# Kernel optimization log

Measured on AMD Instinct MI355X. Metric: run time of the kernel, lower is better.

Reference implementation:

```python
import jax, jax.numpy as jnp
import numpy as np

V, E, H, D, DFF, NB, C, B, T = 32000, 512, 256, 512, 2048, 4, 16, 32, 512
PAD, BOS, EOS = 0, 1, 2


def positional_encoding(t, d):
    pos = jnp.arange(t, dtype=jnp.float32)[:, None]
    i = jnp.arange(0, d, 2, dtype=jnp.float32)
    div = jnp.exp(-(jnp.log(10000.0)) * i / d)
    pe = jnp.zeros((t, d), jnp.float32)
    pe = pe.at[:, 0::2].set(jnp.sin(pos * div))
    pe = pe.at[:, 1::2].set(jnp.cos(pos * div))
    return pe


def layernorm(x, g, b, eps=1e-5):
    mu = jnp.mean(x, -1, keepdims=True)
    var = jnp.mean((x - mu) ** 2, -1, keepdims=True)
    return (x - mu) * jax.lax.rsqrt(var + eps) * g + b


def gru_dir(xs, w_ih, w_hh, b_ih, b_hh, reverse):
    # xs: (B,T,E); precompute input projections for all t (one big GEMM)
    gi = jnp.einsum('bte,ge->btg', xs, w_ih) + b_ih  # (B,T,3H)
    h0 = jnp.zeros((xs.shape[0], H), xs.dtype)

    def step(h, gi_t):
        gh = h @ w_hh.T + b_hh
        i_r, i_z, i_n = jnp.split(gi_t, 3, -1)
        h_r, h_z, h_n = jnp.split(gh, 3, -1)
        r = jax.nn.sigmoid(i_r + h_r)
        z = jax.nn.sigmoid(i_z + h_z)
        n = jnp.tanh(i_n + r * h_n)
        h_new = (1.0 - z) * n + z * h
        return h_new, h_new

    _, hs = jax.lax.scan(step, h0, jnp.swapaxes(gi, 0, 1), reverse=reverse)
    return jnp.swapaxes(hs, 0, 1)  # (B,T,H)


def forward(x, y, embed_W, w_ih_f, w_hh_f, b_ih_f, b_hh_f, w_ih_b, w_hh_b, b_ih_b, b_hh_b,
            ff_w1, ff_b1, ff_w2, ff_b2, ln_g, ln_b, fc_w, fc_b, trans):
    h = embed_W[x]                                   # (B,T,E)
    h = h + positional_encoding(h.shape[1], E)[None]
    hf = gru_dir(h, w_ih_f, w_hh_f, b_ih_f, b_hh_f, False)
    hb = gru_dir(h, w_ih_b, w_hh_b, b_ih_b, b_hh_b, True)
    h = jnp.concatenate([hf, hb], -1)                # (B,T,D)
    for i in range(NB):                              # FeedForward blocks (residual + LN)
        ff = jax.nn.relu(h @ ff_w1[i] + ff_b1[i]) @ ff_w2[i] + ff_b2[i]
        h = layernorm(h + ff, ln_g[i], ln_b[i])
    logits = h @ fc_w + fc_b                         # (B,T,C) emissions

    # --- CRF viterbi decode ---
    mask = (y != PAD)                                # (B,T) bool
    emit = jnp.swapaxes(logits, 0, 1)                # (T,B,C)
    m = jnp.swapaxes(mask, 0, 1)                     # (T,B)
    score0 = trans[BOS][None] + emit[0]              # (B,C)

    def vstep(score, inp):
        e_t, m_t = inp                               # (B,C), (B,)
        cand = score[:, :, None] + trans[None] + e_t[:, None, :]  # (B,prev,cur)
        new = jnp.max(cand, axis=1)
        bp = jnp.argmax(cand, axis=1)                # (B,C)
        new = jnp.where(m_t[:, None], new, score)
        return new, bp

    final, bps = jax.lax.scan(vstep, score0, (emit[1:], m[1:]))  # bps: (T-1,B,C)
    final = final + trans[:, EOS][None]
    best_score = jnp.max(final, -1)                  # (B,)
    last_tag = jnp.argmax(final, -1)                 # (B,)

    def back(tag, inp):
        bp_t, m_t = inp
        prev = jnp.take_along_axis(bp_t, tag[:, None], axis=1)[:, 0]
        prev = jnp.where(m_t, prev, tag)
        return prev, tag

    first_tag, rest = jax.lax.scan(back, last_tag, (bps, m[1:]), reverse=True)
    path = jnp.swapaxes(jnp.concatenate([first_tag[None], rest], 0), 0, 1)  # (B,T)
    return best_score, path


def setup_inputs():
    key = jax.random.key(0)
    ks = jax.random.split(key, 16)
    nrm = lambda k, sh, sc: jax.random.normal(k, sh, jnp.float32) * sc
    s = 1.0 / float(np.sqrt(H))
    inp = {}
    inp['x'] = jax.random.randint(ks[0], (B, T), 1, V)
    inp['y'] = jax.random.randint(ks[1], (B, T), 0, 13) + 3  # in [3,16): no pad/bos/eos
    inp['embed_W'] = nrm(ks[2], (V, E), 0.02)
    inp['w_ih_f'] = nrm(ks[3], (3 * H, E), s); inp['w_hh_f'] = nrm(ks[4], (3 * H, H), s)
    inp['b_ih_f'] = nrm(ks[5], (3 * H,), s); inp['b_hh_f'] = nrm(ks[6], (3 * H,), s)
    inp['w_ih_b'] = nrm(ks[7], (3 * H, E), s); inp['w_hh_b'] = nrm(ks[8], (3 * H, H), s)
    inp['b_ih_b'] = nrm(ks[9], (3 * H,), s); inp['b_hh_b'] = nrm(ks[10], (3 * H,), s)
    inp['ff_w1'] = nrm(ks[11], (NB, D, DFF), 1.0 / float(np.sqrt(D)))
    inp['ff_b1'] = jnp.zeros((NB, DFF), jnp.float32)
    inp['ff_w2'] = nrm(ks[12], (NB, DFF, D), 1.0 / float(np.sqrt(DFF)))
    inp['ff_b2'] = jnp.zeros((NB, D), jnp.float32)
    inp['ln_g'] = jnp.ones((NB, D), jnp.float32); inp['ln_b'] = jnp.zeros((NB, D), jnp.float32)
    inp['fc_w'] = nrm(ks[13], (D, C), 1.0 / float(np.sqrt(D)))
    inp['fc_b'] = jnp.zeros((C,), jnp.float32)
    inp['trans'] = nrm(ks[14], (C, C), 0.1)
    return inp


def reference(x, y, embed_W, w_ih_f, w_hh_f, b_ih_f, b_hh_f, w_ih_b, w_hh_b, b_ih_b, b_hh_b,
              ff_w1, ff_b1, ff_w2, ff_b2, ln_g, ln_b, fc_w, fc_b, trans):
    return forward(x, y, embed_W, w_ih_f, w_hh_f, b_ih_f, b_hh_f, w_ih_b, w_hh_b, b_ih_b, b_hh_b,
                   ff_w1, ff_b1, ff_w2, ff_b2, ln_g, ln_b, fc_w, fc_b, trans)
```

## Files before the change

kernel.cpp:

```cpp
#include <hip/hip_runtime.h>

#define DEV __device__ __forceinline__

using short8 = __attribute__((ext_vector_type(8))) short;
using f32x4  = __attribute__((ext_vector_type(4))) float;
using i32x4  = __attribute__((ext_vector_type(4))) int;

DEV float b2f(short s) {
  union { unsigned u; float f; } c;
  c.u = ((unsigned)(unsigned short)s) << 16;
  return c.f;
}
DEV short f2b(float f) {
  union { float f; unsigned u; } c; c.f = f;
  unsigned u = c.u + 0x7fffu + ((c.u >> 16) & 1u);
  return (short)(u >> 16);
}
DEV float fast_sigmoid(float x) {
  return __builtin_amdgcn_rcpf(1.f + __expf(-x));
}
DEV float fast_tanh(float x) {
  return 1.f - 2.f * __builtin_amdgcn_rcpf(1.f + __expf(2.f * x));
}
DEV void async_ld16(const void* g, void* lds) {
  __builtin_amdgcn_global_load_lds(
      (const __attribute__((address_space(1))) void*)(unsigned long long)g,
      (__attribute__((address_space(3))) void*)(unsigned)(unsigned long long)lds,
      16, 0, 0);
}

__global__ __launch_bounds__(256) void k_cvt2(const float* __restrict__ a, const float* __restrict__ b,
                                              short* __restrict__ oa, short* __restrict__ ob) {
  int blk = blockIdx.x;
  const float* in; short* out; int base;
  if (blk < 384) { in = a; out = oa; base = blk; }
  else           { in = b; out = ob; base = blk - 384; }
  int i = base * 256 + threadIdx.x;
  f32x4 v = *(const f32x4*)(in + (size_t)i * 4);
  short4 o;
#pragma unroll
  for (int j = 0; j < 4; j++) ((short*)&o)[j] = f2b(v[j]);
  *(short4*)(out + (size_t)i * 4) = o;
}

__global__ __launch_bounds__(256) void k_wq8(const float* __restrict__ wf,
                                             const float* __restrict__ wb,
                                             int* __restrict__ out) {
  int flat = blockIdx.x * 256 + threadIdx.x;
  int lane = flat & 63;
  int c = (flat >> 6) & 3;
  int t = flat >> 8;
  int g = t % 3;
  int t2 = t / 3;
  int v = t2 & 15, d = t2 >> 4;
  const float* w = d ? wb : wf;
  int row = g * 256 + v * 16 + (lane & 15);
  int k0 = c * 64 + (lane >> 4) * 16;
  const float* p = w + (size_t)row * 256 + k0;
  int pk[4];
#pragma unroll
  for (int i = 0; i < 4; i++) {
    f32x4 f = *(const f32x4*)(p + i * 4);
    int b0 = (int)__builtin_rintf(f[0] * 256.f);
    int b1 = (int)__builtin_rintf(f[1] * 256.f);
    int b2 = (int)__builtin_rintf(f[2] * 256.f);
    int b3 = (int)__builtin_rintf(f[3] * 256.f);
    b0 = min(127, max(-127, b0)); b1 = min(127, max(-127, b1));
    b2 = min(127, max(-127, b2)); b3 = min(127, max(-127, b3));
    pk[i] = (b0 & 255) | ((b1 & 255) << 8) | ((b2 & 255) << 16) | ((b3 & 255) << 24);
  }
  *(int4*)(out + (size_t)flat * 4) = *(int4*)pk;
}

__global__ __launch_bounds__(256) void k_embed(const int* __restrict__ x,
                                               const float* __restrict__ W,
                                               short* __restrict__ h0) {
  int flat = blockIdx.x * 256 + threadIdx.x;
  int row  = flat >> 6;
  int e0   = (flat & 63) << 3;
  int tok  = x[row];
  int t    = row & 511;
  const float* wp = W + (size_t)tok * 512 + e0;
  float v[8];
  *(f32x4*)v       = *(const f32x4*)(wp);
  *(f32x4*)(v + 4) = *(const f32x4*)(wp + 4);
  short8 o;
#pragma unroll
  for (int i = 0; i < 8; i += 2) {
    float f = expf(-9.210340371976184f * (float)(e0 + i) * (1.f / 512.f));
    float ang = (float)t * f;
    o[i]     = f2b(v[i]     + sinf(ang));
    o[i + 1] = f2b(v[i + 1] + cosf(ang));
  }
  *(short8*)(h0 + (size_t)flat * 8) = o;
}

template <int MODE>
__global__ __launch_bounds__(256) void k_gemm(const short* __restrict__ A,
    const short* __restrict__ B, const float* __restrict__ bias,
    const float* __restrict__ bias2,
    float* __restrict__ Cf, short* __restrict__ Cb, int M, int N, int K,
    const float* __restrict__ tw1, const float* __restrict__ tw2,
    short* __restrict__ w1t, short* __restrict__ w2t) {
  __shared__ __align__(16) char smem[32768];
  short* smA = (short*)smem;
  short* smB = (short*)smem + 8192;
  const int blk0 = blockIdx.x;

  if (MODE == 3 && blk0 >= 1536) {
    int tileid = blk0 - 1536;
    const float* in; short* out; int R, C, tm;
    if (tileid < 4096) { int mat = tileid >> 10; in = tw1 + (size_t)mat * 1048576;
                         out = w1t + (size_t)mat * 1048576; R = 512; C = 2048; tm = tileid & 1023; }
    else               { int mat = (tileid - 4096) >> 10; in = tw2 + (size_t)mat * 1048576;
                         out = w2t + (size_t)mat * 1048576; R = 2048; C = 512; tm = tileid & 1023; }
    float (*tile)[33] = (float(*)[33])smem;
    int ct = C >> 5;
    int bc = tm % ct, br = tm / ct;
    int r0 = br << 5, c0 = bc << 5;
    for (int i = threadIdx.x; i < 1024; i += 256) {
      int r = i >> 5, c = i & 31;
      tile[r][c] = in[(size_t)(r0 + r) * C + c0 + c];
    }
    __syncthreads();
    for (int i = threadIdx.x; i < 1024; i += 256) {
      int c = i >> 5, r = i & 31;
      out[(size_t)(c0 + c) * R + r0 + r] = f2b(tile[r][c]);
    }
    return;
  }

  const int ngemm = (MODE == 3) ? 1536 : gridDim.x;
  const int blk = (blk0 % 8) * (ngemm >> 3) + (blk0 >> 3);
  const int tid = threadIdx.x, lane = tid & 63, wave = tid >> 6;
  const int m15 = lane & 15, quad = lane >> 4, q8 = quad << 3;
  const int tn = N >> 7;
  const int bm = blk / tn, bn = blk % tn;
  const int wm = wave & 1, wn = wave >> 1;
  const f32x4 z4 = {0.f, 0.f, 0.f, 0.f};
  f32x4 acc[4][4];
#pragma unroll
  for (int i = 0; i < 4; i++)
#pragma unroll
    for (int j = 0; j < 4; j++) acc[i][j] = z4;

  for (int k0 = 0; k0 < K; k0 += 64) {
#pragma unroll
    for (int is = 0; is < 4; is++) {
      int c = is * 4 + wave;
      int mb = c & 7, kb = c >> 3;
      async_ld16(A + (size_t)(bm * 128 + mb * 16 + m15) * K + k0 + kb * 32 + q8, smA + c * 512);
      async_ld16(B + (size_t)(bn * 128 + mb * 16 + m15) * K + k0 + kb * 32 + q8, smB + c * 512);
    }
    __syncthreads();
#pragma unroll
    for (int kk = 0; kk < 2; kk++) {
      short8 af[4], bf[4];
#pragma unroll
      for (int i = 0; i < 4; i++)
        af[i] = *(const short8*)(smA + (kk * 8 + wm * 4 + i) * 512 + lane * 8);
#pragma unroll
      for (int j = 0; j < 4; j++)
        bf[j] = *(const short8*)(smB + (kk * 8 + wn * 4 + j) * 512 + lane * 8);
#pragma unroll
      for (int i = 0; i < 4; i++)
#pragma unroll
        for (int j = 0; j < 4; j++)
          acc[i][j] = __builtin_amdgcn_mfma_f32_16x16x32_bf16(bf[j], af[i], acc[i][j], 0, 0, 0);
    }
    __syncthreads();
  }
#pragma unroll
  for (int j = 0; j < 4; j++) {
    int col0 = bn * 128 + wn * 64 + j * 16 + quad * 4;
    f32x4 bv4;
    if (MODE == 3) {
      const float* bp = (col0 < 768) ? (bias + col0) : (bias2 + (col0 - 768));
      bv4 = *(const f32x4*)bp;
    } else {
      bv4 = *(const f32x4*)(bias + col0);
    }
#pragma unroll
    for (int i = 0; i < 4; i++) {
      int row = bm * 128 + wm * 64 + i * 16 + m15;
      f32x4 v;
#pragma unroll
      for (int r = 0; r < 4; r++) v[r] = acc[i][j][r] + bv4[r];
      if (MODE == 1 || MODE == 4) {
        short4 o;
#pragma unroll
        for (int r = 0; r < 4; r++) {
          float x = v[r];
          if (MODE == 1 && x < 0.f) x = 0.f;
          ((short*)&o)[r] = f2b(x);
        }
        *(short4*)(Cb + (size_t)row * N + col0) = o;
      } else if (MODE == 3) {
        short4 o;
#pragma unroll
        for (int r = 0; r < 4; r++) ((short*)&o)[r] = f2b(v[r]);
        *(short4*)(Cb + ((size_t)((row & 511) * 32 + (row >> 9))) * 1536 + col0) = o;
      } else {
        *(f32x4*)(Cf + (size_t)row * N + col0) = v;
      }
    }
  }
}

__global__ __launch_bounds__(1024) void k_gru(
    const int* __restrict__ wq8,
    const float* __restrict__ bhh_f, const float* __restrict__ bhh_b,
    const short* __restrict__ gi16,
    short* __restrict__ hcat16) {
  __shared__ __align__(16) char hb[2][4096];
  const int blk = blockIdx.x;
  const int d = blk & 1, bg = blk >> 1;
  const int tid = threadIdx.x, lane = tid & 63, v = tid >> 6;
  const int m15 = lane & 15, quad = lane >> 4;
  const int col = v * 16 + m15;
  const int brow = quad;
  const float* bhh = d ? bhh_b : bhh_f;
  const float SCL = 1.f / (127.f * 256.f);

  i32x4 Bq[3][4];
  {
    const i32x4* wp = (const i32x4*)wq8 + (size_t)(d * 16 + v) * (3 * 4 * 64);
#pragma unroll
    for (int g = 0; g < 3; g++)
#pragma unroll
      for (int c = 0; c < 4; c++)
        Bq[g][c] = wp[(g * 4 + c) * 64 + lane];
  }
  float bh[3];
#pragma unroll
  for (int g = 0; g < 3; g++) bh[g] = bhh[g * 256 + col];

  const int sw = (m15 & 7) << 4;
  const int aof0 = m15 * 256 + ((quad * 16 +   0) ^ sw);
  const int aof1 = m15 * 256 + ((quad * 16 +  64) ^ sw);
  const int aof2 = m15 * 256 + ((quad * 16 + 128) ^ sw);
  const int aof3 = m15 * 256 + ((quad * 16 + 192) ^ sw);
  const int wofs = brow * 256 + (col ^ (brow << 4));
  const int idx4 = m15 << 2;

  for (int i = tid; i < 2048; i += 1024) ((int*)hb)[i] = 0;

  const int t0 = d ? 511 : 0;
  const long gdelta = (long)(d ? -1 : 1) * 32 * 1536;
  const long hdelta = (long)(d ? -1 : 1) * 32 * 512;
  const short* gp = gi16 + ((size_t)t0 * 32 + bg * 4 + brow) * 1536 + d * 768 + col;
  short* hflush = hcat16 + ((size_t)t0 * 32 + bg * 4 + brow) * 512 + d * 256 + col;

  float gic0 = b2f(gp[0]), gic1 = b2f(gp[256]), gic2 = b2f(gp[512]);
  gp += gdelta;
  float hprev = 0.f;
  unsigned obuf[4] = {0u, 0u, 0u, 0u};
  const i32x4 zi = {0, 0, 0, 0};
  __syncthreads();

  for (int s = 0; s < 512; s++) {
    if ((s & 7) == 0 && s) {
      short* p = hflush;
#pragma unroll
      for (int k = 0; k < 8; k++) {
        *p = (short)(obuf[k >> 1] >> ((k & 1) * 16));
        p += hdelta;
      }
      hflush += 8 * hdelta;
    }
    short n0 = 0, n1 = 0, n2 = 0;
    if (s < 511) {
      n0 = gp[0]; n1 = gp[256]; n2 = gp[512];
      gp += gdelta;
    }
    const char* hs = hb[s & 1];
    i32x4 Af0 = *(const i32x4*)(hs + aof0);
    i32x4 Af1 = *(const i32x4*)(hs + aof1);
    i32x4 Af2 = *(const i32x4*)(hs + aof2);
    i32x4 Af3 = *(const i32x4*)(hs + aof3);
    i32x4 acc0 = zi, acc1 = zi, acc2 = zi;
    acc0 = __builtin_amdgcn_mfma_i32_16x16x64_i8(Af0, Bq[0][0], acc0, 0, 0, 0);
    acc1 = __builtin_amdgcn_mfma_i32_16x16x64_i8(Af0, Bq[1][0], acc1, 0, 0, 0);
    acc2 = __builtin_amdgcn_mfma_i32_16x16x64_i8(Af0, Bq[2][0], acc2, 0, 0, 0);
    acc0 = __builtin_amdgcn_mfma_i32_16x16x64_i8(Af1, Bq[0][1], acc0, 0, 0, 0);
    acc1 = __builtin_amdgcn_mfma_i32_16x16x64_i8(Af1, Bq[1][1], acc1, 0, 0, 0);
    acc2 = __builtin_amdgcn_mfma_i32_16x16x64_i8(Af1, Bq[2][1], acc2, 0, 0, 0);
    acc0 = __builtin_amdgcn_mfma_i32_16x16x64_i8(Af2, Bq[0][2], acc0, 0, 0, 0);
    acc1 = __builtin_amdgcn_mfma_i32_16x16x64_i8(Af2, Bq[1][2], acc1, 0, 0, 0);
    acc2 = __builtin_amdgcn_mfma_i32_16x16x64_i8(Af2, Bq[2][2], acc2, 0, 0, 0);
    acc0 = __builtin_amdgcn_mfma_i32_16x16x64_i8(Af3, Bq[0][3], acc0, 0, 0, 0);
    acc1 = __builtin_amdgcn_mfma_i32_16x16x64_i8(Af3, Bq[1][3], acc1, 0, 0, 0);
    acc2 = __builtin_amdgcn_mfma_i32_16x16x64_i8(Af3, Bq[2][3], acc2, 0, 0, 0);
    int r0 = __builtin_amdgcn_ds_bpermute(idx4, acc0[0]);
    int r1 = __builtin_amdgcn_ds_bpermute(idx4, acc0[1]);
    int r2 = __builtin_amdgcn_ds_bpermute(idx4, acc0[2]);
    int r3 = __builtin_amdgcn_ds_bpermute(idx4, acc0[3]);
    int z0 = __builtin_amdgcn_ds_bpermute(idx4, acc1[0]);
    int z1 = __builtin_amdgcn_ds_bpermute(idx4, acc1[1]);
    int z2 = __builtin_amdgcn_ds_bpermute(idx4, acc1[2]);
    int z3 = __builtin_amdgcn_ds_bpermute(idx4, acc1[3]);
    int n0i = __builtin_amdgcn_ds_bpermute(idx4, acc2[0]);
    int n1i = __builtin_amdgcn_ds_bpermute(idx4, acc2[1]);
    int n2i = __builtin_amdgcn_ds_bpermute(idx4, acc2[2]);
    int n3i = __builtin_amdgcn_ds_bpermute(idx4, acc2[3]);
    int igr = (quad & 2) ? ((quad & 1) ? r3 : r2) : ((quad & 1) ? r1 : r0);
    int igz = (quad & 2) ? ((quad & 1) ? z3 : z2) : ((quad & 1) ? z1 : z0);
    int ign = (quad & 2) ? ((quad & 1) ? n3i : n2i) : ((quad & 1) ? n1i : n0i);
    float r = fast_sigmoid(fmaf((float)igr, SCL, gic0 + bh[0]));
    float z = fast_sigmoid(fmaf((float)igz, SCL, gic1 + bh[1]));
    float n = fast_tanh(fmaf(r, fmaf((float)ign, SCL, bh[2]), gic2));
    float h = (1.f - z) * n + z * hprev;
    hprev = h;
    int hq = (int)__builtin_rintf(h * 127.f);
    hb[(s + 1) & 1][wofs] = (char)hq;
    unsigned hb16 = (unsigned)(unsigned short)f2b(h);
    int idx = s & 7;
    if ((idx & 1) == 0) obuf[idx >> 1] = hb16;
    else                obuf[idx >> 1] |= hb16 << 16;
    gic0 = b2f(n0); gic1 = b2f(n1); gic2 = b2f(n2);
    __syncthreads();
  }
  {
    short* p = hflush;
#pragma unroll
    for (int k = 0; k < 8; k++) {
      *p = (short)(obuf[k >> 1] >> ((k & 1) * 16));
      p += hdelta;
    }
  }
}

template <int FIRST>
__global__ __launch_bounds__(256) void k_ln(const float* __restrict__ hinf,
    const short* __restrict__ ff16, const float* __restrict__ gw,
    const float* __restrict__ bw, float* __restrict__ hout, short* __restrict__ h16) {
  int row = blockIdx.x * 4 + (threadIdx.x >> 6);
  int lane = threadIdx.x & 63;
  size_t base = (size_t)row * 512 + lane * 8;
  f32x4 x0, x1;
  if (FIRST) {
    short8 hv = *(const short8*)(h16 + base);
#pragma unroll
    for (int i = 0; i < 4; i++) { x0[i] = b2f(hv[i]); x1[i] = b2f(hv[4 + i]); }
  } else {
    x0 = *(const f32x4*)(hinf + base);
    x1 = *(const f32x4*)(hinf + base + 4);
  }
  short8 fv = *(const short8*)(ff16 + base);
#pragma unroll
  for (int i = 0; i < 4; i++) { x0[i] += b2f(fv[i]); x1[i] += b2f(fv[4 + i]); }
  float s = x0[0] + x0[1] + x0[2] + x0[3] + x1[0] + x1[1] + x1[2] + x1[3];
#pragma unroll
  for (int off = 32; off >= 1; off >>= 1) s += __shfl_xor(s, off);
  float mu = s * (1.f / 512.f);
  float vv = 0.f;
#pragma unroll
  for (int i = 0; i < 4; i++) { float d0 = x0[i] - mu, d1 = x1[i] - mu; vv += d0 * d0 + d1 * d1; }
#pragma unroll
  for (int off = 32; off >= 1; off >>= 1) vv += __shfl_xor(vv, off);
  float rs = rsqrtf(vv * (1.f / 512.f) + 1e-5f);
  int e = lane * 8;
  f32x4 g0 = *(const f32x4*)(gw + e), g1 = *(const f32x4*)(gw + e + 4);
  f32x4 bb0 = *(const f32x4*)(bw + e), bb1 = *(const f32x4*)(bw + e + 4);
  f32x4 o0, o1; short8 ob;
#pragma unroll
  for (int i = 0; i < 4; i++) {
    float a = (x0[i] - mu) * rs * g0[i] + bb0[i];
    float b = (x1[i] - mu) * rs * g1[i] + bb1[i];
    o0[i] = a; o1[i] = b; ob[i] = f2b(a); ob[4 + i] = f2b(b);
  }
  *(f32x4*)(hout + base) = o0;
  *(f32x4*)(hout + base + 4) = o1;
  *(short8*)(h16 + base) = ob;
}

__global__ __launch_bounds__(256) void k_fc(const float* __restrict__ h,
    const float* __restrict__ fcw, const float* __restrict__ bias,
    float* __restrict__ logits) {
  int row = blockIdx.x * 4 + (threadIdx.x >> 6);
  int lane = threadIdx.x & 63;
  int c = lane & 15, part = lane >> 4;
  const float* ph = h + (size_t)row * 512 + part * 128;
  const float* pw = fcw + (size_t)part * 128 * 16 + c;
  float acc = 0.f;
#pragma unroll 8
  for (int k = 0; k < 128; k += 4) {
    f32x4 hv = *(const f32x4*)(ph + k);
    acc += hv[0] * pw[(k) * 16] + hv[1] * pw[(k + 1) * 16]
         + hv[2] * pw[(k + 2) * 16] + hv[3] * pw[(k + 3) * 16];
  }
  acc += __shfl_xor(acc, 16);
  acc += __shfl_xor(acc, 32);
  if (part == 0) logits[(size_t)row * 16 + c] = acc + bias[c];
}

__global__ __launch_bounds__(64) void k_crf(const float* __restrict__ logits,
    const int* __restrict__ y, const float* __restrict__ trans,
    float* __restrict__ out) {
  __shared__ unsigned char bp[511][16];
  int b = blockIdx.x, lane = threadIdx.x;
  int cur = lane & 15, g = lane >> 4;
  float trr0 = trans[(4 * g + 0) * 16 + cur];
  float trr1 = trans[(4 * g + 1) * 16 + cur];
  float trr2 = trans[(4 * g + 2) * 16 + cur];
  float trr3 = trans[(4 * g + 3) * 16 + cur];
  const float* lg = logits + (size_t)b * 16;
  const int* yb = y + b * 512;
  float score = trans[16 + cur] + lg[cur];
  float e_next = lg[512 + cur];
  int y_next = yb[1];
  for (int t = 1; t < 512; t++) {
    float e = e_next; int ym = y_next;
    if (t < 511) { e_next = lg[(t + 1) * 512 + cur]; y_next = yb[t + 1]; }
    float s0 = __shfl(score, 4 * g + 0);
    float s1 = __shfl(score, 4 * g + 1);
    float s2 = __shfl(score, 4 * g + 2);
    float s3 = __shfl(score, 4 * g + 3);
    float best = s0 + trr0; int arg = 4 * g;
    float c1 = s1 + trr1; if (c1 > best) { best = c1; arg = 4 * g + 1; }
    float c2 = s2 + trr2; if (c2 > best) { best = c2; arg = 4 * g + 2; }
    float c3 = s3 + trr3; if (c3 > best) { best = c3; arg = 4 * g + 3; }
    float pv = __shfl_xor(best, 16); int pa = __shfl_xor(arg, 16);
    bool take = (lane & 16) ? (pv >= best) : (pv > best);
    if (take) { best = pv; arg = pa; }
    pv = __shfl_xor(best, 32); pa = __shfl_xor(arg, 32);
    take = (lane & 32) ? (pv >= best) : (pv > best);
    if (take) { best = pv; arg = pa; }
    if (lane < 16) bp[t - 1][cur] = (unsigned char)arg;
    float ns = best + e;
    if (ym == 0) ns = score;
    score = ns;
  }
  score += trans[cur * 16 + 2];
  float best = -3.4e38f; int argb = 0;
#pragma unroll
  for (int p = 0; p < 16; p++) {
    float sp = __shfl(score, p);
    if (sp > best) { best = sp; argb = p; }
  }
  __syncthreads();
  if (lane == 0) {
    out[b] = best;
    float* po = out + 32 + (size_t)b * 512;
    int tag = argb;
    po[511] = (float)tag;
    for (int t = 511; t >= 1; t--) {
      int prev = bp[t - 1][tag];
      if (yb[t] == 0) prev = tag;
      po[t - 1] = (float)prev;
      tag = prev;
    }
  }
}

extern "C" void kernel_launch(void* const* d_in, const int* in_sizes, int n_in,
                              void* d_out, int out_size, void* d_ws, size_t ws_size,
                              hipStream_t stream) {
  const int*   x      = (const int*)d_in[0];
  const int*   y      = (const int*)d_in[1];
  const float* embedW = (const float*)d_in[2];
  const float* w_ih_f = (const float*)d_in[3];
  const float* w_hh_f = (const float*)d_in[4];
  const float* b_ih_f = (const float*)d_in[5];
  const float* b_hh_f = (const float*)d_in[6];
  const float* w_ih_b = (const float*)d_in[7];
  const float* w_hh_b = (const float*)d_in[8];
  const float* b_ih_b = (const float*)d_in[9];
  const float* b_hh_b = (const float*)d_in[10];
  const float* ff_w1  = (const float*)d_in[11];
  const float* ff_b1  = (const float*)d_in[12];
  const float* ff_w2  = (const float*)d_in[13];
  const float* ff_b2  = (const float*)d_in[14];
  const float* ln_g   = (const float*)d_in[15];
  const float* ln_b   = (const float*)d_in[16];
  const float* fc_w   = (const float*)d_in[17];
  const float* fc_b   = (const float*)d_in[18];
  const float* trans  = (const float*)d_in[19];
  float* out = (float*)d_out;

  char* ws = (char*)d_ws;
  short* h0     = (short*)(ws + 0);
  short* gi16   = (short*)(ws + 16777216);
  short* mid    = (short*)(ws + 16777216);
  short* ffout16= (short*)(ws + 83886080);
  short* wihf16 = (short*)(ws + 117440512);
  short* wihb16 = (short*)(ws + 118226944);
  int*   wq8    = (int*)  (ws + 119013376);
  short* w1t    = (short*)(ws + 119799808);
  short* w2t    = (short*)(ws + 128188416);
  short* hcat16 = (short*)(ws + 136577024);
  float* hres   = (float*)(ws + 153354240);
  float* logits = (float*)(ws + 186908672);

  k_embed<<<4096, 256, 0, stream>>>(x, embedW, h0);
  k_cvt2<<<768, 256, 0, stream>>>(w_ih_f, w_ih_b, wihf16, wihb16);
  k_wq8<<<96, 256, 0, stream>>>(w_hh_f, w_hh_b, wq8);

  k_gemm<3><<<9728, 256, 0, stream>>>(h0, wihf16, b_ih_f, b_ih_b, nullptr, gi16,
                                      16384, 1536, 512, ff_w1, ff_w2, w1t, w2t);

  k_gru<<<16, 1024, 0, stream>>>(wq8, b_hh_f, b_hh_b, gi16, hcat16);

  for (int i = 0; i < 4; i++) {
    k_gemm<1><<<2048, 256, 0, stream>>>(hcat16, w1t + (size_t)i * 1048576, ff_b1 + i * 2048,
                                        nullptr, nullptr, mid, 16384, 2048, 512,
                                        nullptr, nullptr, nullptr, nullptr);
    k_gemm<4><<<512, 256, 0, stream>>>(mid, w2t + (size_t)i * 1048576, ff_b2 + i * 512,
                                       nullptr, nullptr, ffout16, 16384, 512, 2048,
                                       nullptr, nullptr, nullptr, nullptr);
    if (i == 0)
      k_ln<1><<<4096, 256, 0, stream>>>(nullptr, ffout16, ln_g, ln_b, hres, hcat16);
    else
      k_ln<0><<<4096, 256, 0, stream>>>(hres, ffout16, ln_g + i * 512, ln_b + i * 512, hres, hcat16);
  }
  k_fc<<<4096, 256, 0, stream>>>(hres, fc_w, fc_b, logits);
  k_crf<<<32, 64, 0, stream>>>(logits, y, trans, out);
}
```

Baseline: 1.602 ms.

## Move FF weight transposes into GRU launch and use LDS for accumulator redistribution

The FF weight transpose/convert tiles move out of the input-projection GEMM launch into extra blocks of the GRU kernel, so they can run on CUs left idle by the 16 latency-bound GRU blocks. The GEMM loses its block-index swizzle. Inside the GRU step, twelve ds_bpermute shuffles plus selects are replaced by quad-0 lanes writing accumulators to LDS and every lane reading its gate values back. The LDS path relies on the existing per-step barrier for ordering, and may be less efficient for the GEMM's cache locality or for the serial GRU step.

```diff
diff --git a/kernel.cpp b/kernel.cpp
--- a/kernel.cpp
+++ b/kernel.cpp
@@ -99,39 +99,11 @@
 __global__ __launch_bounds__(256) void k_gemm(const short* __restrict__ A,
     const short* __restrict__ B, const float* __restrict__ bias,
     const float* __restrict__ bias2,
-    float* __restrict__ Cf, short* __restrict__ Cb, int M, int N, int K,
-    const float* __restrict__ tw1, const float* __restrict__ tw2,
-    short* __restrict__ w1t, short* __restrict__ w2t) {
+    float* __restrict__ Cf, short* __restrict__ Cb, int M, int N, int K) {
   __shared__ __align__(16) char smem[32768];
   short* smA = (short*)smem;
   short* smB = (short*)smem + 8192;
-  const int blk0 = blockIdx.x;
-
-  if (MODE == 3 && blk0 >= 1536) {
-    int tileid = blk0 - 1536;
-    const float* in; short* out; int R, C, tm;
-    if (tileid < 4096) { int mat = tileid >> 10; in = tw1 + (size_t)mat * 1048576;
-                         out = w1t + (size_t)mat * 1048576; R = 512; C = 2048; tm = tileid & 1023; }
-    else               { int mat = (tileid - 4096) >> 10; in = tw2 + (size_t)mat * 1048576;
-                         out = w2t + (size_t)mat * 1048576; R = 2048; C = 512; tm = tileid & 1023; }
-    float (*tile)[33] = (float(*)[33])smem;
-    int ct = C >> 5;
-    int bc = tm % ct, br = tm / ct;
-    int r0 = br << 5, c0 = bc << 5;
-    for (int i = threadIdx.x; i < 1024; i += 256) {
-      int r = i >> 5, c = i & 31;
-      tile[r][c] = in[(size_t)(r0 + r) * C + c0 + c];
-    }
-    __syncthreads();
-    for (int i = threadIdx.x; i < 1024; i += 256) {
-      int c = i >> 5, r = i & 31;
-      out[(size_t)(c0 + c) * R + r0 + r] = f2b(tile[r][c]);
-    }
-    return;
-  }
-
-  const int ngemm = (MODE == 3) ? 1536 : gridDim.x;
-  const int blk = (blk0 % 8) * (ngemm >> 3) + (blk0 >> 3);
+  const int blk = blockIdx.x;
   const int tid = threadIdx.x, lane = tid & 63, wave = tid >> 6;
   const int m15 = lane & 15, quad = lane >> 4, q8 = quad << 3;
   const int tn = N >> 7;
@@ -211,11 +183,41 @@
     const int* __restrict__ wq8,
     const float* __restrict__ bhh_f, const float* __restrict__ bhh_b,
     const short* __restrict__ gi16,
-    short* __restrict__ hcat16) {
-  __shared__ __align__(16) char hb[2][4096];
+    short* __restrict__ hcat16,
+    const float* __restrict__ ff_w1, const float* __restrict__ ff_w2,
+    short* __restrict__ w1t, short* __restrict__ w2t) {
+  __shared__ __align__(16) char smem[20992];
   const int blk = blockIdx.x;
+  const int tid = threadIdx.x;
+
+  if (blk >= 16) {
+    int sub = tid >> 8, stid = tid & 255;
+    int tileid = (blk - 16) * 4 + sub;
+    const float* in; short* out; int C, R, tm;
+    if (tileid < 4096) { int mat = tileid >> 10; in = ff_w1 + (size_t)mat * 1048576;
+                         out = w1t + (size_t)mat * 1048576; R = 512; C = 2048; tm = tileid & 1023; }
+    else               { int mat = (tileid - 4096) >> 10; in = ff_w2 + (size_t)mat * 1048576;
+                         out = w2t + (size_t)mat * 1048576; R = 2048; C = 512; tm = tileid & 1023; }
+    float (*tile)[33] = (float(*)[33])(smem + sub * 4224);
+    int ct = C >> 5;
+    int bc = tm % ct, br = tm / ct;
+    int r0 = br << 5, c0 = bc << 5;
+    for (int i = stid; i < 1024; i += 256) {
+      int r = i >> 5, c = i & 31;
+      tile[r][c] = in[(size_t)(r0 + r) * C + c0 + c];
+    }
+    __syncthreads();
+    for (int i = stid; i < 1024; i += 256) {
+      int c = i >> 5, r = i & 31;
+      out[(size_t)(c0 + c) * R + r0 + r] = f2b(tile[r][c]);
+    }
+    return;
+  }
+
+  char (*hb)[4096] = (char(*)[4096])smem;
+  int (*smGi)[200] = (int(*)[200])(smem + 8192);
   const int d = blk & 1, bg = blk >> 1;
-  const int tid = threadIdx.x, lane = tid & 63, v = tid >> 6;
+  const int lane = tid & 63, v = tid >> 6;
   const int m15 = lane & 15, quad = lane >> 4;
   const int col = v * 16 + m15;
   const int brow = quad;
@@ -241,7 +243,6 @@
   const int aof2 = m15 * 256 + ((quad * 16 + 128) ^ sw);
   const int aof3 = m15 * 256 + ((quad * 16 + 192) ^ sw);
   const int wofs = brow * 256 + (col ^ (brow << 4));
-  const int idx4 = m15 << 2;
 
   for (int i = tid; i < 2048; i += 1024) ((int*)hb)[i] = 0;
 
@@ -291,21 +292,17 @@
     acc0 = __builtin_amdgcn_mfma_i32_16x16x64_i8(Af3, Bq[0][3], acc0, 0, 0, 0);
     acc1 = __builtin_amdgcn_mfma_i32_16x16x64_i8(Af3, Bq[1][3], acc1, 0, 0, 0);
     acc2 = __builtin_amdgcn_mfma_i32_16x16x64_i8(Af3, Bq[2][3], acc2, 0, 0, 0);
-    int r0 = __builtin_amdgcn_ds_bpermute(idx4, acc0[0]);
-    int r1 = __builtin_amdgcn_ds_bpermute(idx4, acc0[1]);
-    int r2 = __builtin_amdgcn_ds_bpermute(idx4, acc0[2]);
-    int r3 = __builtin_amdgcn_ds_bpermute(idx4, acc0[3]);
-    int z0 = __builtin_amdgcn_ds_bpermute(idx4, acc1[0]);
-    int z1 = __builtin_amdgcn_ds_bpermute(idx4, acc1[1]);
-    int z2 = __builtin_amdgcn_ds_bpermute(idx4, acc1[2]);
-    int z3 = __builtin_amdgcn_ds_bpermute(idx4, acc1[3]);
-    int n0i = __builtin_amdgcn_ds_bpermute(idx4, acc2[0]);
-    int n1i = __builtin_amdgcn_ds_bpermute(idx4, acc2[1]);
-    int n2i = __builtin_amdgcn_ds_bpermute(idx4, acc2[2]);
-    int n3i = __builtin_amdgcn_ds_bpermute(idx4, acc2[3]);
-    int igr = (quad & 2) ? ((quad & 1) ? r3 : r2) : ((quad & 1) ? r1 : r0);
-    int igz = (quad & 2) ? ((quad & 1) ? z3 : z2) : ((quad & 1) ? z1 : z0);
-    int ign = (quad & 2) ? ((quad & 1) ? n3i : n2i) : ((quad & 1) ? n1i : n0i);
+    if (quad == 0) {
+#pragma unroll
+      for (int i = 0; i < 4; i++) {
+        smGi[v][i * 16 + m15]       = acc0[i];
+        smGi[v][64 + i * 16 + m15]  = acc1[i];
+        smGi[v][128 + i * 16 + m15] = acc2[i];
+      }
+    }
+    int igr = smGi[v][lane];
+    int igz = smGi[v][64 + lane];
+    int ign = smGi[v][128 + lane];
     float r = fast_sigmoid(fmaf((float)igr, SCL, gic0 + bh[0]));
     float z = fast_sigmoid(fmaf((float)igz, SCL, gic1 + bh[1]));
     float n = fast_tanh(fmaf(r, fmaf((float)ign, SCL, bh[2]), gic2));
@@ -496,18 +493,16 @@
   k_cvt2<<<768, 256, 0, stream>>>(w_ih_f, w_ih_b, wihf16, wihb16);
   k_wq8<<<96, 256, 0, stream>>>(w_hh_f, w_hh_b, wq8);
 
-  k_gemm<3><<<9728, 256, 0, stream>>>(h0, wihf16, b_ih_f, b_ih_b, nullptr, gi16,
-                                      16384, 1536, 512, ff_w1, ff_w2, w1t, w2t);
-
-  k_gru<<<16, 1024, 0, stream>>>(wq8, b_hh_f, b_hh_b, gi16, hcat16);
+  k_gemm<3><<<1536, 256, 0, stream>>>(h0, wihf16, b_ih_f, b_ih_b, nullptr, gi16, 16384, 1536, 512);
+
+  k_gru<<<2064, 1024, 0, stream>>>(wq8, b_hh_f, b_hh_b, gi16, hcat16,
+                                   ff_w1, ff_w2, w1t, w2t);
 
   for (int i = 0; i < 4; i++) {
     k_gemm<1><<<2048, 256, 0, stream>>>(hcat16, w1t + (size_t)i * 1048576, ff_b1 + i * 2048,
-                                        nullptr, nullptr, mid, 16384, 2048, 512,
-                                        nullptr, nullptr, nullptr, nullptr);
+                                        nullptr, nullptr, mid, 16384, 2048, 512);
     k_gemm<4><<<512, 256, 0, stream>>>(mid, w2t + (size_t)i * 1048576, ff_b2 + i * 512,
-                                       nullptr, nullptr, ffout16, 16384, 512, 2048,
-                                       nullptr, nullptr, nullptr, nullptr);
+                                       nullptr, nullptr, ffout16, 16384, 512, 2048);
     if (i == 0)
       k_ln<1><<<4096, 256, 0, stream>>>(nullptr, ffout16, ln_g, ln_b, hres, hcat16);
     else
```

New measurement: 1.526 ms. 4.8% less time.
